# Kernel tuning notes

Measured on AMD Instinct MI355X. Metric: run time of the kernel, lower is better.

## Reference

```python
import jax, jax.numpy as jnp
import numpy as np

B_, CIN, HH, WW = 2, 64, 64, 64
D_MODEL, D_INNER, D_STATE, DT_RANK, D_CONV = 64, 128, 16, 32, 3


def setup_inputs() -> dict:
    key = jax.random.key(0)
    ks = jax.random.split(key, 16)
    w = lambda k, shape: jax.random.normal(k, shape, jnp.float32) * 0.05
    # dt_proj bias init (torch: inv-softplus of dt sampled in [dt_min, dt_max])
    dt = jnp.exp(jax.random.uniform(ks[10], (D_INNER,)) * (np.log(0.1) - np.log(0.001)) + np.log(0.001))
    dt = jnp.clip(dt, 1e-4, None)
    inv_dt = dt + jnp.log(-jnp.expm1(-dt))
    A = jnp.tile(jnp.arange(1, D_STATE + 1, dtype=jnp.float32), (D_INNER, 1))
    return {
        "rgb_feat": jax.random.normal(ks[0], (B_, CIN, HH, WW), jnp.float32),
        "dte_feat": jax.random.normal(ks[1], (B_, CIN, HH, WW), jnp.float32),
        "conv1_w": w(ks[2], (D_MODEL, CIN)), "conv1_b": jnp.zeros((D_MODEL,), jnp.float32),
        "conv2_w": w(ks[3], (D_MODEL, CIN)), "conv2_b": jnp.zeros((D_MODEL,), jnp.float32),
        "conv3_w": w(ks[4], (CIN, D_MODEL)), "conv3_b": jnp.zeros((CIN,), jnp.float32),
        "norm_w": jnp.ones((D_MODEL,), jnp.float32),
        "in_proj_w": w(ks[5], (2 * D_INNER, D_MODEL)),
        "conv1d_w": w(ks[6], (D_INNER, D_CONV)), "conv1d_b": jnp.zeros((D_INNER,), jnp.float32),
        "x_proj_w": w(ks[7], (DT_RANK + 2 * D_STATE, D_INNER)),
        "dt_proj_w": jax.random.uniform(ks[8], (D_INNER, DT_RANK), jnp.float32, -DT_RANK ** -0.5, DT_RANK ** -0.5),
        "dt_proj_b": inv_dt,
        "A_log": jnp.log(A),
        "Dp": jnp.ones((D_INNER,), jnp.float32),
        "out_proj_w": w(ks[9], (D_MODEL, D_INNER)),
    }


def _conv1x1(x, w, b):
    return jnp.einsum('bchw,oc->bohw', x, w) + b[None, :, None, None]


def _rmsnorm(x, w, eps=1e-5):
    return x * jax.lax.rsqrt(jnp.mean(x * x, axis=-1, keepdims=True) + eps) * w


def _dwconv1d(x, w, b):
    # x: [B,L,D]; depthwise conv, kernel 3, padding 1 (same length)
    xt = jnp.transpose(x, (0, 2, 1))  # [B,D,L]
    y = jax.lax.conv_general_dilated(xt, w[:, None, :], (1,), [(1, 1)],
                                     dimension_numbers=('NCH', 'OIH', 'NCH'),
                                     feature_group_count=D_INNER)
    return jnp.transpose(y + b[None, :, None], (0, 2, 1))


def _mamba(x, h, p):
    # x: [B,L,d_model]
    xz = x @ p['in_proj_w'].T                      # [B,L,2*d_inner]
    xc, z = jnp.split(xz, 2, axis=-1)
    xc = jax.nn.silu(_dwconv1d(xc, p['conv1d_w'], p['conv1d_b']))
    A = -jnp.exp(p['A_log'])                       # [D,S]
    dbc = xc @ p['x_proj_w'].T                     # [B,L,dt_rank+2S]
    delta, Bm, Cm = jnp.split(dbc, [DT_RANK, DT_RANK + D_STATE], axis=-1)
    delta = jax.nn.softplus(delta @ p['dt_proj_w'].T + p['dt_proj_b'])  # [B,L,D]
    deltaA = jnp.exp(delta[..., None] * A)         # [B,L,D,S]
    BX = delta[..., None] * Bm[:, :, None, :] * xc[..., None]  # [B,L,D,S]
    h = deltaA * h + BX
    y = jnp.einsum('blds,bls->bld', h, Cm) + p['Dp'] * xc
    out = (y * jax.nn.silu(z)) @ p['out_proj_w'].T
    return out, h


def _residual_block(x4d, h, p):
    B, C, H, W = x4d.shape
    x = jnp.transpose(x4d.reshape(B, C, H * W), (0, 2, 1))  # [B,L,C]
    x = _rmsnorm(x, p['norm_w'])
    out, h = _mamba(x, h, p)
    out = out + x
    return jnp.transpose(out, (0, 2, 1)).reshape(B, C, H, W), h


def _rsfm(rgb_feat, dte_feat, conv1_w, conv1_b, conv2_w, conv2_b, conv3_w, conv3_b,
          norm_w, in_proj_w, conv1d_w, conv1d_b, x_proj_w, dt_proj_w, dt_proj_b,
          A_log, Dp, out_proj_w):
    p = dict(norm_w=norm_w, in_proj_w=in_proj_w, conv1d_w=conv1d_w, conv1d_b=conv1d_b,
             x_proj_w=x_proj_w, dt_proj_w=dt_proj_w, dt_proj_b=dt_proj_b,
             A_log=A_log, Dp=Dp, out_proj_w=out_proj_w)
    rgb = _conv1x1(rgb_feat, conv1_w, conv1_b)
    dte = _conv1x1(dte_feat, conv2_w, conv2_b)
    B = rgb.shape[0]
    h = jnp.zeros((B, HH * WW, D_INNER, D_STATE), jnp.float32)
    out1, h = _residual_block(rgb, h, p)
    out2, h = _residual_block(dte + out1, h, p)
    out3, h = _residual_block(rgb + out2, h, p)
    out4, h = _residual_block(dte + out3, h, p)
    out5, h = _residual_block(rgb + out4, h, p)
    out6, h = _residual_block(dte + out5, h, p)
    return _conv1x1(out6, conv3_w, conv3_b), h


def reference(rgb_feat, dte_feat, conv1_w, conv1_b, conv2_w, conv2_b, conv3_w, conv3_b,
              norm_w, in_proj_w, conv1d_w, conv1d_b, x_proj_w, dt_proj_w, dt_proj_b,
              A_log, Dp, out_proj_w):
    return _rsfm(rgb_feat, dte_feat, conv1_w, conv1_b, conv2_w, conv2_b, conv3_w, conv3_b,
                 norm_w, in_proj_w, conv1d_w, conv1d_b, x_proj_w, dt_proj_w, dt_proj_b,
                 A_log, Dp, out_proj_w)
```

## Files before the change

### kernel.cpp

```cpp
#include <hip/hip_runtime.h>

#define LSEQ 4096
#define NPOS 8192

__device__ __forceinline__ float silu_f(float x){ return x / (1.f + __expf(-x)); }
__device__ __forceinline__ float softplus_f(float x){
  return fmaxf(x, 0.f) + log1pf(__expf(-fabsf(x)));
}

__global__ __launch_bounds__(256) void k_prep(
    const float* __restrict__ ipw, const float* __restrict__ xpw,
    const float* __restrict__ dtw, const float* __restrict__ opw,
    const float* __restrict__ w1, const float* __restrict__ w2,
    const float* __restrict__ w3, const float* __restrict__ alog,
    float* __restrict__ ipT, float* __restrict__ xpT,
    float* __restrict__ dtT, float* __restrict__ opT,
    float* __restrict__ w1T, float* __restrict__ w2T,
    float* __restrict__ w3T, float* __restrict__ Aneg)
{
  int t = blockIdx.x * 256 + threadIdx.x;
  if (t < 16384){ int o = t >> 6, c = t & 63; ipT[c * 256 + o] = ipw[t]; }
  if (t < 8192){ int o = t >> 7, d = t & 127; xpT[d * 64 + o] = xpw[t]; }
  if (t < 4096){ int d = t >> 5, r = t & 31; dtT[r * 128 + d] = dtw[t]; }
  if (t < 8192){ int o = t >> 7, d = t & 127; opT[d * 64 + o] = opw[t]; }
  if (t < 4096){ int o = t >> 6, c = t & 63;
                 w1T[c*64+o] = w1[t]; w2T[c*64+o] = w2[t]; w3T[c*64+o] = w3[t]; }
  if (t < 2048){ Aneg[t] = -__expf(alog[t]); }
}

__global__ __launch_bounds__(256) void k_convin(
    const float* __restrict__ rgb, const float* __restrict__ dte,
    const float* __restrict__ w1T, const float* __restrict__ b1,
    const float* __restrict__ w2T, const float* __restrict__ b2,
    float* __restrict__ rgbp, float* __restrict__ dtep)
{
  int gw = (blockIdx.x * 256 + threadIdx.x) >> 6;
  int lane = threadIdx.x & 63;
  int which = gw >> 13;
  int n = gw & 8191;
  const float* x  = which ? dte : rgb;
  const float* wT = which ? w2T : w1T;
  const float* bb = which ? b2 : b1;
  float* o = which ? dtep : rgbp;
  int b = n >> 12, l = n & 4095;
  const float* xp = x + (size_t)b * 262144 + l;
  float acc = bb[lane];
  for (int c = 0; c < 64; c++)
    acc += wT[c*64 + lane] * xp[(size_t)c * 4096];
  o[(size_t)n*64 + lane] = acc;
}

__global__ __launch_bounds__(256) void k_pre(
    const float* __restrict__ xin, const float* __restrict__ normw,
    const float* __restrict__ ipT,
    float* __restrict__ xn, float* __restrict__ xcp, float* __restrict__ zs)
{
  __shared__ __align__(16) float xnl[4][8][64];
  const int wv = threadIdx.x >> 6, lane = threadIdx.x & 63;
  const int n0 = (blockIdx.x * 4 + wv) * 8;
  float nw = normw[lane];
  #pragma unroll 1
  for (int p = 0; p < 8; p++){
    int n = n0 + p;
    float v = xin[(size_t)n*64 + lane];
    float ss = v * v;
    for (int m = 32; m > 0; m >>= 1) ss += __shfl_xor(ss, m);
    v = v * rsqrtf(ss * (1.f/64.f) + 1e-5f) * nw;
    xn[(size_t)n*64 + lane] = v;
    xnl[wv][p][lane] = v;
  }
  float ac[8][4] = {};
  for (int c = 0; c < 64; c++){
    float w0 = ipT[c*256 + lane],       w1 = ipT[c*256 + 64 + lane];
    float w2 = ipT[c*256 + 128 + lane], w3 = ipT[c*256 + 192 + lane];
    #pragma unroll
    for (int p = 0; p < 8; p++){
      float xv = xnl[wv][p][c];
      ac[p][0] += w0*xv; ac[p][1] += w1*xv; ac[p][2] += w2*xv; ac[p][3] += w3*xv;
    }
  }
  #pragma unroll
  for (int p = 0; p < 8; p++){
    int n = n0 + p;
    xcp[(size_t)n*128 + lane]      = ac[p][0];
    xcp[(size_t)n*128 + 64 + lane] = ac[p][1];
    zs[(size_t)n*128 + lane]       = silu_f(ac[p][2]);
    zs[(size_t)n*128 + 64 + lane]  = silu_f(ac[p][3]);
  }
}

__global__ __launch_bounds__(256) void k_step(
    const float* __restrict__ xcpA, float* __restrict__ xcpB,
    float* __restrict__ zs, float* __restrict__ xn,
    float* __restrict__ h, const float* __restrict__ base_next,
    const float* __restrict__ xpT, const float* __restrict__ dtT,
    const float* __restrict__ opT, const float* __restrict__ Aneg,
    const float* __restrict__ c1w, const float* __restrict__ c1b,
    const float* __restrict__ dtb, const float* __restrict__ Dpw,
    const float* __restrict__ normw, const float* __restrict__ ipT,
    int hasH, int fusePre)
{
  __shared__ __align__(16) float xcl[4][4][128];
  __shared__ __align__(16) float dbl[4][4][64];
  __shared__ __align__(16) float yzl[4][4][128];
  __shared__ __align__(16) float xnl[4][4][64];
  const int wv = threadIdx.x >> 6, lane = threadIdx.x & 63;
  const int n0 = (blockIdx.x * 4 + wv) * 4;
  const int d0 = lane, d1 = 64 + lane;

  float cw00 = c1w[d0*3+0], cw01 = c1w[d0*3+1], cw02 = c1w[d0*3+2];
  float cw10 = c1w[d1*3+0], cw11 = c1w[d1*3+1], cw12 = c1w[d1*3+2];
  float cb0 = c1b[d0], cb1 = c1b[d1];

  float xc[4][2];
  #pragma unroll
  for (int p = 0; p < 4; p++){
    int n = n0 + p, l = n & (LSEQ-1);
    const float* xr = xcpA + (size_t)n * 128;
    float am0 = (l > 0) ? xr[d0 - 128] : 0.f;
    float am1 = (l > 0) ? xr[d1 - 128] : 0.f;
    float a00 = xr[d0], a01 = xr[d1];
    float ap0 = (l < LSEQ-1) ? xr[d0 + 128] : 0.f;
    float ap1 = (l < LSEQ-1) ? xr[d1 + 128] : 0.f;
    float v0 = silu_f(cw00*am0 + cw01*a00 + cw02*ap0 + cb0);
    float v1 = silu_f(cw10*am1 + cw11*a01 + cw12*ap1 + cb1);
    xc[p][0] = v0; xc[p][1] = v1;
    xcl[wv][p][d0] = v0; xcl[wv][p][d1] = v1;
  }

  float xa0=0.f, xa1=0.f, xa2=0.f, xa3=0.f;
  for (int d = 0; d < 128; d++){
    float w = xpT[d*64 + lane];
    xa0 += w * xcl[wv][0][d];
    xa1 += w * xcl[wv][1][d];
    xa2 += w * xcl[wv][2][d];
    xa3 += w * xcl[wv][3][d];
  }
  dbl[wv][0][lane]=xa0; dbl[wv][1][lane]=xa1; dbl[wv][2][lane]=xa2; dbl[wv][3][lane]=xa3;

  float tb0 = dtb[d0], tb1 = dtb[d1];
  float da[4][2];
  #pragma unroll
  for (int p = 0; p < 4; p++){ da[p][0]=tb0; da[p][1]=tb1; }
  for (int r = 0; r < 32; r++){
    float w0 = dtT[r*128 + d0];
    float w1 = dtT[r*128 + d1];
    #pragma unroll
    for (int p = 0; p < 4; p++){
      float bv = dbl[wv][p][r];
      da[p][0] += w0 * bv; da[p][1] += w1 * bv;
    }
  }
  float dl[4][2];
  #pragma unroll
  for (int p = 0; p < 4; p++){ dl[p][0]=softplus_f(da[p][0]); dl[p][1]=softplus_f(da[p][1]); }

  float an0[16], an1[16];
  {
    const float4* A0 = (const float4*)(Aneg + d0*16);
    const float4* A1 = (const float4*)(Aneg + d1*16);
    #pragma unroll
    for (int q = 0; q < 4; q++){
      float4 a = A0[q]; an0[q*4+0]=a.x; an0[q*4+1]=a.y; an0[q*4+2]=a.z; an0[q*4+3]=a.w;
      float4 b = A1[q]; an1[q*4+0]=b.x; an1[q*4+1]=b.y; an1[q*4+2]=b.z; an1[q*4+3]=b.w;
    }
  }
  float dp0 = Dpw[d0], dp1 = Dpw[d1];

  #pragma unroll 1
  for (int p = 0; p < 4; p++){
    int n = n0 + p;
    float Bm[16], Cm[16];
    {
      const float4* bb = (const float4*)&dbl[wv][p][32];
      const float4* cc = (const float4*)&dbl[wv][p][48];
      #pragma unroll
      for (int q = 0; q < 4; q++){
        float4 a = bb[q]; Bm[q*4+0]=a.x; Bm[q*4+1]=a.y; Bm[q*4+2]=a.z; Bm[q*4+3]=a.w;
        float4 b = cc[q]; Cm[q*4+0]=b.x; Cm[q*4+1]=b.y; Cm[q*4+2]=b.z; Cm[q*4+3]=b.w;
      }
    }
    float* hp0 = h + ((size_t)n*2048 + (size_t)d0*16);
    float* hp1 = h + ((size_t)n*2048 + (size_t)d1*16);
    float h0[16], h1[16];
    if (hasH){
      #pragma unroll
      for (int q = 0; q < 4; q++){
        float4 v = ((const float4*)hp0)[q];
        h0[q*4+0]=v.x; h0[q*4+1]=v.y; h0[q*4+2]=v.z; h0[q*4+3]=v.w;
        float4 w = ((const float4*)hp1)[q];
        h1[q*4+0]=w.x; h1[q*4+1]=w.y; h1[q*4+2]=w.z; h1[q*4+3]=w.w;
      }
    } else {
      #pragma unroll
      for (int s = 0; s < 16; s++){ h0[s]=0.f; h1[s]=0.f; }
    }
    float y0 = 0.f, y1 = 0.f;
    float dl0 = dl[p][0], dl1 = dl[p][1];
    float bx0 = dl0 * xc[p][0], bx1 = dl1 * xc[p][1];
    #pragma unroll
    for (int s = 0; s < 16; s++){
      h0[s] = __expf(dl0*an0[s])*h0[s] + bx0*Bm[s];
      y0 += h0[s]*Cm[s];
      h1[s] = __expf(dl1*an1[s])*h1[s] + bx1*Bm[s];
      y1 += h1[s]*Cm[s];
    }
    #pragma unroll
    for (int q = 0; q < 4; q++){
      float4 v; v.x=h0[q*4+0]; v.y=h0[q*4+1]; v.z=h0[q*4+2]; v.w=h0[q*4+3];
      ((float4*)hp0)[q] = v;
      float4 w; w.x=h1[q*4+0]; w.y=h1[q*4+1]; w.z=h1[q*4+2]; w.w=h1[q*4+3];
      ((float4*)hp1)[q] = w;
    }
    y0 += dp0 * xc[p][0];
    y1 += dp1 * xc[p][1];
    yzl[wv][p][d0] = y0 * zs[(size_t)n*128 + d0];
    yzl[wv][p][d1] = y1 * zs[(size_t)n*128 + d1];
  }

  float oa[4] = {0.f,0.f,0.f,0.f};
  for (int d = 0; d < 128; d++){
    float w = opT[d*64 + lane];
    oa[0] += w * yzl[wv][0][d];
    oa[1] += w * yzl[wv][1][d];
    oa[2] += w * yzl[wv][2][d];
    oa[3] += w * yzl[wv][3][d];
  }

  float nw = normw[lane];
  if (fusePre){
    #pragma unroll 1
    for (int p = 0; p < 4; p++){
      int n = n0 + p;
      float v = oa[p] + xn[(size_t)n*64 + lane] + base_next[(size_t)n*64 + lane];
      float ss = v * v;
      for (int m = 32; m > 0; m >>= 1) ss += __shfl_xor(ss, m);
      v = v * rsqrtf(ss * (1.f/64.f) + 1e-5f) * nw;
      xn[(size_t)n*64 + lane] = v;
      xnl[wv][p][lane] = v;
    }
    float ac[4][4] = {};
    for (int c = 0; c < 64; c++){
      float w0 = ipT[c*256 + lane],       w1 = ipT[c*256 + 64 + lane];
      float w2 = ipT[c*256 + 128 + lane], w3 = ipT[c*256 + 192 + lane];
      #pragma unroll
      for (int p = 0; p < 4; p++){
        float xv = xnl[wv][p][c];
        ac[p][0] += w0*xv; ac[p][1] += w1*xv; ac[p][2] += w2*xv; ac[p][3] += w3*xv;
      }
    }
    #pragma unroll
    for (int p = 0; p < 4; p++){
      int n = n0 + p;
      xcpB[(size_t)n*128 + lane]      = ac[p][0];
      xcpB[(size_t)n*128 + 64 + lane] = ac[p][1];
      zs[(size_t)n*128 + lane]        = silu_f(ac[p][2]);
      zs[(size_t)n*128 + 64 + lane]   = silu_f(ac[p][3]);
    }
  } else {
    #pragma unroll
    for (int p = 0; p < 4; p++){
      int n = n0 + p;
      xcpB[(size_t)n*64 + lane] = oa[p] + xn[(size_t)n*64 + lane];
    }
  }
}

__global__ __launch_bounds__(256) void k_conv3(
    const float* __restrict__ out6, const float* __restrict__ w3T,
    const float* __restrict__ b3, float* __restrict__ out)
{
  __shared__ __align__(16) float t[64][65];
  const int tid = threadIdx.x;
  const int n0 = blockIdx.x * 64;
  #pragma unroll
  for (int i = 0; i < 16; i++){
    int idx = tid + 256*i;
    int r = idx >> 6, c = idx & 63;
    t[r][c] = out6[(size_t)(n0 + r)*64 + c];
  }
  __syncthreads();
  const int i = tid & 63;
  const int cb = (tid >> 6) * 16;
  float acc[16];
  #pragma unroll
  for (int j = 0; j < 16; j++) acc[j] = b3[cb + j];
  for (int o = 0; o < 64; o++){
    float xv = t[i][o];
    #pragma unroll
    for (int j = 0; j < 16; j++) acc[j] += w3T[o*64 + cb + j] * xv;
  }
  const int b = n0 >> 12;
  const int l = (n0 & 4095) + i;
  #pragma unroll
  for (int j = 0; j < 16; j++)
    out[(size_t)b*262144 + (size_t)(cb + j)*4096 + l] = acc[j];
}

extern "C" void kernel_launch(void* const* d_in, const int* in_sizes, int n_in,
                              void* d_out, int out_size, void* d_ws, size_t ws_size,
                              hipStream_t stream)
{
  const float* rgb  = (const float*)d_in[0];
  const float* dte  = (const float*)d_in[1];
  const float* w1   = (const float*)d_in[2];
  const float* b1   = (const float*)d_in[3];
  const float* w2   = (const float*)d_in[4];
  const float* b2   = (const float*)d_in[5];
  const float* w3   = (const float*)d_in[6];
  const float* b3   = (const float*)d_in[7];
  const float* nrm  = (const float*)d_in[8];
  const float* ipw  = (const float*)d_in[9];
  const float* c1w  = (const float*)d_in[10];
  const float* c1b  = (const float*)d_in[11];
  const float* xpw  = (const float*)d_in[12];
  const float* dtw  = (const float*)d_in[13];
  const float* dtb  = (const float*)d_in[14];
  const float* alog = (const float*)d_in[15];
  const float* Dpw  = (const float*)d_in[16];
  const float* opw  = (const float*)d_in[17];

  float* out  = (float*)d_out;
  float* hbuf = out + 524288;

  float* ws   = (float*)d_ws;
  float* rgbp = ws;
  float* dtep = ws + 524288;
  float* xnb  = ws + 1048576;
  float* zsb  = ws + 1572864;
  float* xcp0 = ws + 2621440;
  float* xcp1 = ws + 3670016;
  float* Aneg = ws + 4718592;
  float* wb   = ws + 4720640;
  float* ipT = wb;
  float* xpT = wb + 16384;
  float* dtT = wb + 24576;
  float* opT = wb + 28672;
  float* w1T = wb + 36864;
  float* w2T = wb + 40960;
  float* w3T = wb + 45056;

  k_prep<<<64, 256, 0, stream>>>(ipw, xpw, dtw, opw, w1, w2, w3, alog,
                                 ipT, xpT, dtT, opT, w1T, w2T, w3T, Aneg);
  k_convin<<<4096, 256, 0, stream>>>(rgb, dte, w1T, b1, w2T, b2, rgbp, dtep);
  k_pre<<<256, 256, 0, stream>>>(rgbp, nrm, ipT, xnb, xcp0, zsb);

  float* xa[2] = {xcp0, xcp1};
  for (int k = 0; k < 6; k++){
    const float* base = (k == 5) ? nullptr : ((k & 1) ? rgbp : dtep);
    k_step<<<512, 256, 0, stream>>>(xa[k & 1], xa[(k & 1) ^ 1], zsb, xnb, hbuf, base,
                                    xpT, dtT, opT, Aneg, c1w, c1b, dtb, Dpw, nrm, ipT,
                                    (k > 0) ? 1 : 0, (k < 5) ? 1 : 0);
  }
  k_conv3<<<128, 256, 0, stream>>>(xcp0, w3T, b3, out);
}
```

Baseline: 417.4 us.

## Fuse whole pipeline into one persistent kernel with grid barriers

Replaces the input conv, pre-projection, six residual step launches and final conv with one persistent kernel of 512 blocks. Blocks synchronise through an atomic grid barrier only where the depthwise conv needs neighbouring positions. The SSM state, normalised activations and gate values stay in registers across all six blocks, so the per-step global reads and writes of h, xn and zs go away and h is written once at the end. In exchange the kernel carries a large register footprint and needs all 512 blocks resident at once, or the spin barrier with its timeout break can give wrong results.

Result: slower. 1.070 ms (+156.3%).

```diff
diff --git a/kernel.cpp b/kernel.cpp
--- a/kernel.cpp
+++ b/kernel.cpp
@@ -2,10 +2,27 @@
 
 #define LSEQ 4096
 #define NPOS 8192
+#define NBLK 512
 
 __device__ __forceinline__ float silu_f(float x){ return x / (1.f + __expf(-x)); }
 __device__ __forceinline__ float softplus_f(float x){
   return fmaxf(x, 0.f) + log1pf(__expf(-fabsf(x)));
+}
+
+__device__ __forceinline__ void gsync(unsigned* bar, int slot){
+  __syncthreads();
+  if (threadIdx.x == 0){
+    __threadfence();
+    atomicAdd(&bar[slot], 1u);
+    int guard = 0;
+    while (__hip_atomic_load(&bar[slot], __ATOMIC_ACQUIRE,
+                             __HIP_MEMORY_SCOPE_AGENT) < (unsigned)NBLK){
+      __builtin_amdgcn_s_sleep(2);
+      if (++guard > (1 << 22)) break;
+    }
+    __threadfence();
+  }
+  __syncthreads();
 }
 
 __global__ __launch_bounds__(256) void k_prep(
@@ -28,273 +45,243 @@
   if (t < 2048){ Aneg[t] = -__expf(alog[t]); }
 }
 
-__global__ __launch_bounds__(256) void k_convin(
+__global__ __launch_bounds__(256, 2) void k_fused(
     const float* __restrict__ rgb, const float* __restrict__ dte,
-    const float* __restrict__ w1T, const float* __restrict__ b1,
-    const float* __restrict__ w2T, const float* __restrict__ b2,
-    float* __restrict__ rgbp, float* __restrict__ dtep)
-{
-  int gw = (blockIdx.x * 256 + threadIdx.x) >> 6;
-  int lane = threadIdx.x & 63;
-  int which = gw >> 13;
-  int n = gw & 8191;
-  const float* x  = which ? dte : rgb;
-  const float* wT = which ? w2T : w1T;
-  const float* bb = which ? b2 : b1;
-  float* o = which ? dtep : rgbp;
-  int b = n >> 12, l = n & 4095;
-  const float* xp = x + (size_t)b * 262144 + l;
-  float acc = bb[lane];
-  for (int c = 0; c < 64; c++)
-    acc += wT[c*64 + lane] * xp[(size_t)c * 4096];
-  o[(size_t)n*64 + lane] = acc;
-}
-
-__global__ __launch_bounds__(256) void k_pre(
-    const float* __restrict__ xin, const float* __restrict__ normw,
-    const float* __restrict__ ipT,
-    float* __restrict__ xn, float* __restrict__ xcp, float* __restrict__ zs)
-{
-  __shared__ __align__(16) float xnl[4][8][64];
-  const int wv = threadIdx.x >> 6, lane = threadIdx.x & 63;
-  const int n0 = (blockIdx.x * 4 + wv) * 8;
-  float nw = normw[lane];
-  #pragma unroll 1
-  for (int p = 0; p < 8; p++){
-    int n = n0 + p;
-    float v = xin[(size_t)n*64 + lane];
-    float ss = v * v;
-    for (int m = 32; m > 0; m >>= 1) ss += __shfl_xor(ss, m);
-    v = v * rsqrtf(ss * (1.f/64.f) + 1e-5f) * nw;
-    xn[(size_t)n*64 + lane] = v;
-    xnl[wv][p][lane] = v;
-  }
-  float ac[8][4] = {};
-  for (int c = 0; c < 64; c++){
-    float w0 = ipT[c*256 + lane],       w1 = ipT[c*256 + 64 + lane];
-    float w2 = ipT[c*256 + 128 + lane], w3 = ipT[c*256 + 192 + lane];
-    #pragma unroll
-    for (int p = 0; p < 8; p++){
-      float xv = xnl[wv][p][c];
-      ac[p][0] += w0*xv; ac[p][1] += w1*xv; ac[p][2] += w2*xv; ac[p][3] += w3*xv;
-    }
-  }
-  #pragma unroll
-  for (int p = 0; p < 8; p++){
-    int n = n0 + p;
-    xcp[(size_t)n*128 + lane]      = ac[p][0];
-    xcp[(size_t)n*128 + 64 + lane] = ac[p][1];
-    zs[(size_t)n*128 + lane]       = silu_f(ac[p][2]);
-    zs[(size_t)n*128 + 64 + lane]  = silu_f(ac[p][3]);
-  }
-}
-
-__global__ __launch_bounds__(256) void k_step(
-    const float* __restrict__ xcpA, float* __restrict__ xcpB,
-    float* __restrict__ zs, float* __restrict__ xn,
-    float* __restrict__ h, const float* __restrict__ base_next,
+    const float* __restrict__ b1, const float* __restrict__ b2,
+    const float* __restrict__ w1T, const float* __restrict__ w2T,
+    const float* __restrict__ normw, const float* __restrict__ ipT,
     const float* __restrict__ xpT, const float* __restrict__ dtT,
     const float* __restrict__ opT, const float* __restrict__ Aneg,
     const float* __restrict__ c1w, const float* __restrict__ c1b,
     const float* __restrict__ dtb, const float* __restrict__ Dpw,
-    const float* __restrict__ normw, const float* __restrict__ ipT,
-    int hasH, int fusePre)
+    const float* __restrict__ w3T, const float* __restrict__ b3,
+    float* __restrict__ xcp0, float* __restrict__ xcp1,
+    unsigned* __restrict__ bar,
+    float* __restrict__ outc, float* __restrict__ hout)
 {
+  __shared__ __align__(16) float inT[2][64][16];
   __shared__ __align__(16) float xcl[4][4][128];
   __shared__ __align__(16) float dbl[4][4][64];
   __shared__ __align__(16) float yzl[4][4][128];
   __shared__ __align__(16) float xnl[4][4][64];
+  __shared__ __align__(16) float o6l[16][65];
+
   const int wv = threadIdx.x >> 6, lane = threadIdx.x & 63;
-  const int n0 = (blockIdx.x * 4 + wv) * 4;
+  const int nb = blockIdx.x * 16;
+  const int b  = nb >> 12, l0 = nb & 4095;
+  const int n0 = nb + wv * 4;
   const int d0 = lane, d1 = 64 + lane;
 
-  float cw00 = c1w[d0*3+0], cw01 = c1w[d0*3+1], cw02 = c1w[d0*3+2];
-  float cw10 = c1w[d1*3+0], cw11 = c1w[d1*3+1], cw12 = c1w[d1*3+2];
-  float cb0 = c1b[d0], cb1 = c1b[d1];
-
-  float xc[4][2];
+  #pragma unroll
+  for (int j = 0; j < 8; j++){
+    int e = threadIdx.x + 256 * j;
+    int w = e >> 10, c = (e >> 4) & 63, p = e & 15;
+    const float* src = w ? dte : rgb;
+    inT[w][c][p] = src[(size_t)b * 262144 + (size_t)c * 4096 + l0 + p];
+  }
+  __syncthreads();
+
+  float bR[4], bD[4];
+  {
+    float aR[4], aD[4];
+    float biR = b1[lane], biD = b2[lane];
+    #pragma unroll
+    for (int p = 0; p < 4; p++){ aR[p] = biR; aD[p] = biD; }
+    for (int c = 0; c < 64; c++){
+      float wr = w1T[c*64 + lane], wd = w2T[c*64 + lane];
+      #pragma unroll
+      for (int p = 0; p < 4; p++){
+        aR[p] += wr * inT[0][c][wv*4 + p];
+        aD[p] += wd * inT[1][c][wv*4 + p];
+      }
+    }
+    #pragma unroll
+    for (int p = 0; p < 4; p++){ bR[p] = aR[p]; bD[p] = aD[p]; }
+  }
+
+  const float nw = normw[lane];
+  const float cw00 = c1w[d0*3+0], cw01 = c1w[d0*3+1], cw02 = c1w[d0*3+2];
+  const float cw10 = c1w[d1*3+0], cw11 = c1w[d1*3+1], cw12 = c1w[d1*3+2];
+  const float cb0 = c1b[d0], cb1 = c1b[d1];
+  const float tb0 = dtb[d0], tb1 = dtb[d1];
+  const float dp0 = Dpw[d0], dp1 = Dpw[d1];
+
+  float xn[4], zs0[4], zs1[4];
+  float h0[4][16], h1[4][16];
+  #pragma unroll
+  for (int p = 0; p < 4; p++)
+    #pragma unroll
+    for (int s = 0; s < 16; s++){ h0[p][s] = 0.f; h1[p][s] = 0.f; }
+
   #pragma unroll
   for (int p = 0; p < 4; p++){
-    int n = n0 + p, l = n & (LSEQ-1);
-    const float* xr = xcpA + (size_t)n * 128;
-    float am0 = (l > 0) ? xr[d0 - 128] : 0.f;
-    float am1 = (l > 0) ? xr[d1 - 128] : 0.f;
-    float a00 = xr[d0], a01 = xr[d1];
-    float ap0 = (l < LSEQ-1) ? xr[d0 + 128] : 0.f;
-    float ap1 = (l < LSEQ-1) ? xr[d1 + 128] : 0.f;
-    float v0 = silu_f(cw00*am0 + cw01*a00 + cw02*ap0 + cb0);
-    float v1 = silu_f(cw10*am1 + cw11*a01 + cw12*ap1 + cb1);
-    xc[p][0] = v0; xc[p][1] = v1;
-    xcl[wv][p][d0] = v0; xcl[wv][p][d1] = v1;
-  }
-
-  float xa0=0.f, xa1=0.f, xa2=0.f, xa3=0.f;
-  for (int d = 0; d < 128; d++){
-    float w = xpT[d*64 + lane];
-    xa0 += w * xcl[wv][0][d];
-    xa1 += w * xcl[wv][1][d];
-    xa2 += w * xcl[wv][2][d];
-    xa3 += w * xcl[wv][3][d];
-  }
-  dbl[wv][0][lane]=xa0; dbl[wv][1][lane]=xa1; dbl[wv][2][lane]=xa2; dbl[wv][3][lane]=xa3;
-
-  float tb0 = dtb[d0], tb1 = dtb[d1];
-  float da[4][2];
-  #pragma unroll
-  for (int p = 0; p < 4; p++){ da[p][0]=tb0; da[p][1]=tb1; }
-  for (int r = 0; r < 32; r++){
-    float w0 = dtT[r*128 + d0];
-    float w1 = dtT[r*128 + d1];
-    #pragma unroll
-    for (int p = 0; p < 4; p++){
-      float bv = dbl[wv][p][r];
-      da[p][0] += w0 * bv; da[p][1] += w1 * bv;
-    }
-  }
-  float dl[4][2];
-  #pragma unroll
-  for (int p = 0; p < 4; p++){ dl[p][0]=softplus_f(da[p][0]); dl[p][1]=softplus_f(da[p][1]); }
-
-  float an0[16], an1[16];
+    float v = bR[p];
+    float ss = v * v;
+    for (int m = 32; m > 0; m >>= 1) ss += __shfl_xor(ss, m);
+    v = v * rsqrtf(ss * (1.f/64.f) + 1e-5f) * nw;
+    xn[p] = v; xnl[wv][p][lane] = v;
+  }
   {
-    const float4* A0 = (const float4*)(Aneg + d0*16);
-    const float4* A1 = (const float4*)(Aneg + d1*16);
-    #pragma unroll
-    for (int q = 0; q < 4; q++){
-      float4 a = A0[q]; an0[q*4+0]=a.x; an0[q*4+1]=a.y; an0[q*4+2]=a.z; an0[q*4+3]=a.w;
-      float4 b = A1[q]; an1[q*4+0]=b.x; an1[q*4+1]=b.y; an1[q*4+2]=b.z; an1[q*4+3]=b.w;
-    }
-  }
-  float dp0 = Dpw[d0], dp1 = Dpw[d1];
-
-  #pragma unroll 1
-  for (int p = 0; p < 4; p++){
-    int n = n0 + p;
-    float Bm[16], Cm[16];
-    {
-      const float4* bb = (const float4*)&dbl[wv][p][32];
-      const float4* cc = (const float4*)&dbl[wv][p][48];
-      #pragma unroll
-      for (int q = 0; q < 4; q++){
-        float4 a = bb[q]; Bm[q*4+0]=a.x; Bm[q*4+1]=a.y; Bm[q*4+2]=a.z; Bm[q*4+3]=a.w;
-        float4 b = cc[q]; Cm[q*4+0]=b.x; Cm[q*4+1]=b.y; Cm[q*4+2]=b.z; Cm[q*4+3]=b.w;
-      }
-    }
-    float* hp0 = h + ((size_t)n*2048 + (size_t)d0*16);
-    float* hp1 = h + ((size_t)n*2048 + (size_t)d1*16);
-    float h0[16], h1[16];
-    if (hasH){
-      #pragma unroll
-      for (int q = 0; q < 4; q++){
-        float4 v = ((const float4*)hp0)[q];
-        h0[q*4+0]=v.x; h0[q*4+1]=v.y; h0[q*4+2]=v.z; h0[q*4+3]=v.w;
-        float4 w = ((const float4*)hp1)[q];
-        h1[q*4+0]=w.x; h1[q*4+1]=w.y; h1[q*4+2]=w.z; h1[q*4+3]=w.w;
-      }
-    } else {
-      #pragma unroll
-      for (int s = 0; s < 16; s++){ h0[s]=0.f; h1[s]=0.f; }
-    }
-    float y0 = 0.f, y1 = 0.f;
-    float dl0 = dl[p][0], dl1 = dl[p][1];
-    float bx0 = dl0 * xc[p][0], bx1 = dl1 * xc[p][1];
-    #pragma unroll
-    for (int s = 0; s < 16; s++){
-      h0[s] = __expf(dl0*an0[s])*h0[s] + bx0*Bm[s];
-      y0 += h0[s]*Cm[s];
-      h1[s] = __expf(dl1*an1[s])*h1[s] + bx1*Bm[s];
-      y1 += h1[s]*Cm[s];
-    }
-    #pragma unroll
-    for (int q = 0; q < 4; q++){
-      float4 v; v.x=h0[q*4+0]; v.y=h0[q*4+1]; v.z=h0[q*4+2]; v.w=h0[q*4+3];
-      ((float4*)hp0)[q] = v;
-      float4 w; w.x=h1[q*4+0]; w.y=h1[q*4+1]; w.z=h1[q*4+2]; w.w=h1[q*4+3];
-      ((float4*)hp1)[q] = w;
-    }
-    y0 += dp0 * xc[p][0];
-    y1 += dp1 * xc[p][1];
-    yzl[wv][p][d0] = y0 * zs[(size_t)n*128 + d0];
-    yzl[wv][p][d1] = y1 * zs[(size_t)n*128 + d1];
-  }
-
-  float oa[4] = {0.f,0.f,0.f,0.f};
-  for (int d = 0; d < 128; d++){
-    float w = opT[d*64 + lane];
-    oa[0] += w * yzl[wv][0][d];
-    oa[1] += w * yzl[wv][1][d];
-    oa[2] += w * yzl[wv][2][d];
-    oa[3] += w * yzl[wv][3][d];
-  }
-
-  float nw = normw[lane];
-  if (fusePre){
-    #pragma unroll 1
+    float aX0[4] = {0,0,0,0}, aX1[4] = {0,0,0,0};
+    float aZ0[4] = {0,0,0,0}, aZ1[4] = {0,0,0,0};
+    for (int c = 0; c < 64; c++){
+      float wx0 = ipT[c*256 + lane],       wx1 = ipT[c*256 + 64 + lane];
+      float wz0 = ipT[c*256 + 128 + lane], wz1 = ipT[c*256 + 192 + lane];
+      #pragma unroll
+      for (int p = 0; p < 4; p++){
+        float xv = xnl[wv][p][c];
+        aX0[p] += wx0*xv; aX1[p] += wx1*xv; aZ0[p] += wz0*xv; aZ1[p] += wz1*xv;
+      }
+    }
+    #pragma unroll
     for (int p = 0; p < 4; p++){
       int n = n0 + p;
-      float v = oa[p] + xn[(size_t)n*64 + lane] + base_next[(size_t)n*64 + lane];
-      float ss = v * v;
-      for (int m = 32; m > 0; m >>= 1) ss += __shfl_xor(ss, m);
-      v = v * rsqrtf(ss * (1.f/64.f) + 1e-5f) * nw;
-      xn[(size_t)n*64 + lane] = v;
-      xnl[wv][p][lane] = v;
-    }
-    float ac[4][4] = {};
-    for (int c = 0; c < 64; c++){
-      float w0 = ipT[c*256 + lane],       w1 = ipT[c*256 + 64 + lane];
-      float w2 = ipT[c*256 + 128 + lane], w3 = ipT[c*256 + 192 + lane];
-      #pragma unroll
-      for (int p = 0; p < 4; p++){
-        float xv = xnl[wv][p][c];
-        ac[p][0] += w0*xv; ac[p][1] += w1*xv; ac[p][2] += w2*xv; ac[p][3] += w3*xv;
-      }
-    }
+      xcp0[(size_t)n*128 + lane]      = aX0[p];
+      xcp0[(size_t)n*128 + 64 + lane] = aX1[p];
+      zs0[p] = silu_f(aZ0[p]); zs1[p] = silu_f(aZ1[p]);
+    }
+  }
+  gsync(bar, 0);
+
+  const float4* A4 = (const float4*)Aneg;
+  #pragma unroll 1
+  for (int k = 0; k < 6; k++){
+    const float* xA = (k & 1) ? xcp1 : xcp0;
+    float*       xB = (k & 1) ? xcp0 : xcp1;
+
+    float xc0[4], xc1[4];
     #pragma unroll
     for (int p = 0; p < 4; p++){
-      int n = n0 + p;
-      xcpB[(size_t)n*128 + lane]      = ac[p][0];
-      xcpB[(size_t)n*128 + 64 + lane] = ac[p][1];
-      zs[(size_t)n*128 + lane]        = silu_f(ac[p][2]);
-      zs[(size_t)n*128 + 64 + lane]   = silu_f(ac[p][3]);
-    }
-  } else {
+      int n = n0 + p, l = n & 4095;
+      const float* xr = xA + (size_t)n * 128;
+      float am0 = 0.f, am1 = 0.f, ap0 = 0.f, ap1 = 0.f;
+      if (l > 0)    { am0 = xr[d0 - 128]; am1 = xr[d1 - 128]; }
+      float a00 = xr[d0], a01 = xr[d1];
+      if (l < 4095) { ap0 = xr[d0 + 128]; ap1 = xr[d1 + 128]; }
+      float v0 = silu_f(cw00*am0 + cw01*a00 + cw02*ap0 + cb0);
+      float v1 = silu_f(cw10*am1 + cw11*a01 + cw12*ap1 + cb1);
+      xc0[p] = v0; xc1[p] = v1;
+      xcl[wv][p][d0] = v0; xcl[wv][p][d1] = v1;
+    }
+
+    {
+      float xa[4] = {0,0,0,0};
+      for (int d = 0; d < 128; d++){
+        float w = xpT[d*64 + lane];
+        #pragma unroll
+        for (int p = 0; p < 4; p++) xa[p] += w * xcl[wv][p][d];
+      }
+      #pragma unroll
+      for (int p = 0; p < 4; p++) dbl[wv][p][lane] = xa[p];
+    }
+
+    float dl0[4], dl1[4];
+    {
+      float da0[4], da1[4];
+      #pragma unroll
+      for (int p = 0; p < 4; p++){ da0[p] = tb0; da1[p] = tb1; }
+      for (int r = 0; r < 32; r++){
+        float w0 = dtT[r*128 + d0], w1 = dtT[r*128 + d1];
+        #pragma unroll
+        for (int p = 0; p < 4; p++){
+          float bv = dbl[wv][p][r];
+          da0[p] += w0 * bv; da1[p] += w1 * bv;
+        }
+      }
+      #pragma unroll
+      for (int p = 0; p < 4; p++){ dl0[p] = softplus_f(da0[p]); dl1[p] = softplus_f(da1[p]); }
+    }
+
     #pragma unroll
     for (int p = 0; p < 4; p++){
-      int n = n0 + p;
-      xcpB[(size_t)n*64 + lane] = oa[p] + xn[(size_t)n*64 + lane];
-    }
-  }
-}
-
-__global__ __launch_bounds__(256) void k_conv3(
-    const float* __restrict__ out6, const float* __restrict__ w3T,
-    const float* __restrict__ b3, float* __restrict__ out)
-{
-  __shared__ __align__(16) float t[64][65];
-  const int tid = threadIdx.x;
-  const int n0 = blockIdx.x * 64;
-  #pragma unroll
-  for (int i = 0; i < 16; i++){
-    int idx = tid + 256*i;
-    int r = idx >> 6, c = idx & 63;
-    t[r][c] = out6[(size_t)(n0 + r)*64 + c];
-  }
-  __syncthreads();
-  const int i = tid & 63;
-  const int cb = (tid >> 6) * 16;
-  float acc[16];
-  #pragma unroll
-  for (int j = 0; j < 16; j++) acc[j] = b3[cb + j];
-  for (int o = 0; o < 64; o++){
-    float xv = t[i][o];
-    #pragma unroll
-    for (int j = 0; j < 16; j++) acc[j] += w3T[o*64 + cb + j] * xv;
-  }
-  const int b = n0 >> 12;
-  const int l = (n0 & 4095) + i;
-  #pragma unroll
-  for (int j = 0; j < 16; j++)
-    out[(size_t)b*262144 + (size_t)(cb + j)*4096 + l] = acc[j];
+      float y0 = 0.f, y1 = 0.f;
+      float bx0 = dl0[p] * xc0[p], bx1 = dl1[p] * xc1[p];
+      #pragma unroll
+      for (int q = 0; q < 4; q++){
+        float4 a0 = A4[d0*4 + q];
+        float4 a1 = A4[d1*4 + q];
+        float4 bq = *(const float4*)&dbl[wv][p][32 + q*4];
+        float4 cq = *(const float4*)&dbl[wv][p][48 + q*4];
+        h0[p][q*4+0] = __expf(dl0[p]*a0.x)*h0[p][q*4+0] + bx0*bq.x; y0 = fmaf(h0[p][q*4+0], cq.x, y0);
+        h0[p][q*4+1] = __expf(dl0[p]*a0.y)*h0[p][q*4+1] + bx0*bq.y; y0 = fmaf(h0[p][q*4+1], cq.y, y0);
+        h0[p][q*4+2] = __expf(dl0[p]*a0.z)*h0[p][q*4+2] + bx0*bq.z; y0 = fmaf(h0[p][q*4+2], cq.z, y0);
+        h0[p][q*4+3] = __expf(dl0[p]*a0.w)*h0[p][q*4+3] + bx0*bq.w; y0 = fmaf(h0[p][q*4+3], cq.w, y0);
+        h1[p][q*4+0] = __expf(dl1[p]*a1.x)*h1[p][q*4+0] + bx1*bq.x; y1 = fmaf(h1[p][q*4+0], cq.x, y1);
+        h1[p][q*4+1] = __expf(dl1[p]*a1.y)*h1[p][q*4+1] + bx1*bq.y; y1 = fmaf(h1[p][q*4+1], cq.y, y1);
+        h1[p][q*4+2] = __expf(dl1[p]*a1.z)*h1[p][q*4+2] + bx1*bq.z; y1 = fmaf(h1[p][q*4+2], cq.z, y1);
+        h1[p][q*4+3] = __expf(dl1[p]*a1.w)*h1[p][q*4+3] + bx1*bq.w; y1 = fmaf(h1[p][q*4+3], cq.w, y1);
+      }
+      y0 += dp0 * xc0[p];
+      y1 += dp1 * xc1[p];
+      yzl[wv][p][d0] = y0 * zs0[p];
+      yzl[wv][p][d1] = y1 * zs1[p];
+    }
+
+    float oa[4] = {0,0,0,0};
+    for (int d = 0; d < 128; d++){
+      float w = opT[d*64 + lane];
+      #pragma unroll
+      for (int p = 0; p < 4; p++) oa[p] += w * yzl[wv][p][d];
+    }
+
+    if (k < 5){
+      #pragma unroll
+      for (int p = 0; p < 4; p++){
+        float v = oa[p] + xn[p] + ((k & 1) ? bR[p] : bD[p]);
+        float ss = v * v;
+        for (int m = 32; m > 0; m >>= 1) ss += __shfl_xor(ss, m);
+        v = v * rsqrtf(ss * (1.f/64.f) + 1e-5f) * nw;
+        xn[p] = v; xnl[wv][p][lane] = v;
+      }
+      float aX0[4] = {0,0,0,0}, aX1[4] = {0,0,0,0};
+      float aZ0[4] = {0,0,0,0}, aZ1[4] = {0,0,0,0};
+      for (int c = 0; c < 64; c++){
+        float wx0 = ipT[c*256 + lane],       wx1 = ipT[c*256 + 64 + lane];
+        float wz0 = ipT[c*256 + 128 + lane], wz1 = ipT[c*256 + 192 + lane];
+        #pragma unroll
+        for (int p = 0; p < 4; p++){
+          float xv = xnl[wv][p][c];
+          aX0[p] += wx0*xv; aX1[p] += wx1*xv; aZ0[p] += wz0*xv; aZ1[p] += wz1*xv;
+        }
+      }
+      #pragma unroll
+      for (int p = 0; p < 4; p++){
+        int n = n0 + p;
+        xB[(size_t)n*128 + lane]      = aX0[p];
+        xB[(size_t)n*128 + 64 + lane] = aX1[p];
+        zs0[p] = silu_f(aZ0[p]); zs1[p] = silu_f(aZ1[p]);
+      }
+      gsync(bar, k + 1);
+    } else {
+      #pragma unroll
+      for (int p = 0; p < 4; p++){
+        int n = n0 + p;
+        float4* hp0 = (float4*)(hout + (size_t)n*2048 + (size_t)d0*16);
+        float4* hp1 = (float4*)(hout + (size_t)n*2048 + (size_t)d1*16);
+        #pragma unroll
+        for (int q = 0; q < 4; q++){
+          float4 v; v.x=h0[p][q*4+0]; v.y=h0[p][q*4+1]; v.z=h0[p][q*4+2]; v.w=h0[p][q*4+3];
+          hp0[q] = v;
+          float4 w; w.x=h1[p][q*4+0]; w.y=h1[p][q*4+1]; w.z=h1[p][q*4+2]; w.w=h1[p][q*4+3];
+          hp1[q] = w;
+        }
+        o6l[wv*4 + p][lane] = oa[p] + xn[p];
+      }
+      __syncthreads();
+      int o  = threadIdx.x >> 2;
+      int pb = (threadIdx.x & 3) * 4;
+      float ac0 = b3[o], ac1 = ac0, ac2 = ac0, ac3 = ac0;
+      for (int c = 0; c < 64; c++){
+        float w = w3T[c*64 + o];
+        ac0 += w * o6l[pb + 0][c];
+        ac1 += w * o6l[pb + 1][c];
+        ac2 += w * o6l[pb + 2][c];
+        ac3 += w * o6l[pb + 3][c];
+      }
+      size_t ob = (size_t)b * 262144 + (size_t)o * 4096 + l0 + pb;
+      outc[ob + 0] = ac0; outc[ob + 1] = ac1; outc[ob + 2] = ac2; outc[ob + 3] = ac3;
+    }
+  }
 }
 
 extern "C" void kernel_launch(void* const* d_in, const int* in_sizes, int n_in,
@@ -320,37 +307,27 @@
   const float* Dpw  = (const float*)d_in[16];
   const float* opw  = (const float*)d_in[17];
 
-  float* out  = (float*)d_out;
-  float* hbuf = out + 524288;
+  float* outc = (float*)d_out;
+  float* hout = outc + 524288;
 
   float* ws   = (float*)d_ws;
-  float* rgbp = ws;
-  float* dtep = ws + 524288;
-  float* xnb  = ws + 1048576;
-  float* zsb  = ws + 1572864;
-  float* xcp0 = ws + 2621440;
-  float* xcp1 = ws + 3670016;
-  float* Aneg = ws + 4718592;
-  float* wb   = ws + 4720640;
-  float* ipT = wb;
-  float* xpT = wb + 16384;
-  float* dtT = wb + 24576;
-  float* opT = wb + 28672;
-  float* w1T = wb + 36864;
-  float* w2T = wb + 40960;
-  float* w3T = wb + 45056;
-
+  float* xcp0 = ws;
+  float* xcp1 = ws + 1048576;
+  float* wb   = ws + 2097152;
+  float* ipT  = wb;
+  float* xpT  = wb + 16384;
+  float* dtT  = wb + 24576;
+  float* opT  = wb + 28672;
+  float* w1T  = wb + 36864;
+  float* w2T  = wb + 40960;
+  float* w3T  = wb + 45056;
+  float* Aneg = wb + 49152;
+  unsigned* bar = (unsigned*)(wb + 51200);
+
+  hipMemsetAsync((void*)bar, 0, 64, stream);
   k_prep<<<64, 256, 0, stream>>>(ipw, xpw, dtw, opw, w1, w2, w3, alog,
                                  ipT, xpT, dtT, opT, w1T, w2T, w3T, Aneg);
-  k_convin<<<4096, 256, 0, stream>>>(rgb, dte, w1T, b1, w2T, b2, rgbp, dtep);
-  k_pre<<<256, 256, 0, stream>>>(rgbp, nrm, ipT, xnb, xcp0, zsb);
-
-  float* xa[2] = {xcp0, xcp1};
-  for (int k = 0; k < 6; k++){
-    const float* base = (k == 5) ? nullptr : ((k & 1) ? rgbp : dtep);
-    k_step<<<512, 256, 0, stream>>>(xa[k & 1], xa[(k & 1) ^ 1], zsb, xnb, hbuf, base,
-                                    xpT, dtT, opT, Aneg, c1w, c1b, dtb, Dpw, nrm, ipT,
-                                    (k > 0) ? 1 : 0, (k < 5) ? 1 : 0);
-  }
-  k_conv3<<<128, 256, 0, stream>>>(xcp0, w3T, b3, out);
-}
+  k_fused<<<NBLK, 256, 0, stream>>>(rgb, dte, b1, b2, w1T, w2T, nrm, ipT,
+                                    xpT, dtT, opT, Aneg, c1w, c1b, dtb, Dpw,
+                                    w3T, b3, xcp0, xcp1, bar, outc, hout);
+}
```
